# Kernel tuning notes

Hardware: AMD Instinct MI355X
Metric: run time of the kernel (lower is better)

Reference implementation:

```python
import jax, jax.numpy as jnp
import numpy as np

HEAD_DIM = 256
HIDDEN = 2560
NUM_HEADS = 8
NUM_KV_HEADS = 4
INPUT_DIM = HIDDEN * 2
B, S = 2, 2048


def rotate_half(x):
    x1, x2 = x[..., : x.shape[-1] // 2], x[..., x.shape[-1] // 2 :]
    return jnp.concatenate((-x2, x1), axis=-1)


def setup_inputs() -> dict:
    key = jax.random.key(0)
    ks = jax.random.split(key, 6)
    hidden_states = jax.random.normal(ks[0], (B, S, INPUT_DIM), dtype=jnp.float32)
    # causal additive mask (0 on/below diagonal, large negative above)
    causal = jnp.tril(jnp.ones((S, S), dtype=bool))
    attention_mask = jnp.where(causal, 0.0, -1e9).astype(jnp.float32)
    attention_mask = jnp.broadcast_to(attention_mask[None, None], (B, 1, S, S))
    position_ids = jnp.broadcast_to(jnp.arange(S, dtype=jnp.int32)[None], (B, S))
    sc = 1.0 / np.sqrt(INPUT_DIM)
    Wq = jax.random.normal(ks[1], (NUM_HEADS * HEAD_DIM, INPUT_DIM), dtype=jnp.float32) * sc
    Wk = jax.random.normal(ks[2], (NUM_KV_HEADS * HEAD_DIM, INPUT_DIM), dtype=jnp.float32) * sc
    Wv = jax.random.normal(ks[3], (NUM_KV_HEADS * HEAD_DIM, INPUT_DIM), dtype=jnp.float32) * sc
    Wo = jax.random.normal(ks[4], (HIDDEN, NUM_HEADS * HEAD_DIM), dtype=jnp.float32) * (1.0 / np.sqrt(NUM_HEADS * HEAD_DIM))
    return {"hidden_states": hidden_states, "attention_mask": attention_mask,
            "position_ids": position_ids, "Wq": Wq, "Wk": Wk, "Wv": Wv, "Wo": Wo}


def reference(hidden_states, attention_mask, position_ids, Wq, Wk, Wv, Wo):
    bsz, q_len, _ = hidden_states.shape
    groups = NUM_HEADS // NUM_KV_HEADS
    q = (hidden_states @ Wq.T).reshape(bsz, q_len, NUM_HEADS, HEAD_DIM).transpose(0, 2, 1, 3)
    k = (hidden_states @ Wk.T).reshape(bsz, q_len, NUM_KV_HEADS, HEAD_DIM).transpose(0, 2, 1, 3)
    v = (hidden_states @ Wv.T).reshape(bsz, q_len, NUM_KV_HEADS, HEAD_DIM).transpose(0, 2, 1, 3)
    # RoPE (uses position_ids[0], matching the torch module)
    inv_freq = 1.0 / (10000.0 ** (jnp.arange(0, HEAD_DIM, 2, dtype=jnp.float32) / HEAD_DIM))
    freqs = position_ids[0].astype(jnp.float32)[:, None] * inv_freq[None, :]  # [S, D/2]
    emb = jnp.concatenate((freqs, freqs), axis=-1)  # [S, D]
    cos = jnp.cos(emb)[None, None].astype(q.dtype)
    sin = jnp.sin(emb)[None, None].astype(q.dtype)
    q = q * cos + rotate_half(q) * sin
    k = k * cos + rotate_half(k) * sin
    # GQA: repeat kv heads
    k = jnp.repeat(k, groups, axis=1)  # [B, H, S, D]
    v = jnp.repeat(v, groups, axis=1)
    scores = jnp.einsum("bhqd,bhkd->bhqk", q, k) / np.sqrt(HEAD_DIM)
    scores = scores + attention_mask
    attn = jax.nn.softmax(scores.astype(jnp.float32), axis=-1).astype(q.dtype)
    out = jnp.einsum("bhqk,bhkd->bhqd", attn, v)
    out = out.transpose(0, 2, 1, 3).reshape(bsz, q_len, NUM_HEADS * HEAD_DIM)
    return out @ Wo.T
```

## Files before the change

### kernel.cpp

```cpp
#include <hip/hip_runtime.h>
#include <hip/hip_bf16.h>
#include <cstdint>
#include <cstddef>

typedef __bf16 bf16;
typedef bf16 bf16x4 __attribute__((ext_vector_type(4)));
typedef bf16 bf16x8 __attribute__((ext_vector_type(8)));
typedef float f32x4 __attribute__((ext_vector_type(4)));

#define HEAD_DIM 256
#define NHEADS 8
#define NKV 4
#define BATCH 2
#define SEQ 2048
#define IND 5120
#define HID 2560
#define ROWS (BATCH*SEQ)
#define NQKV 4096
#define CHUNKS_PER_BH 80

__device__ __forceinline__ f32x4 mfma16(bf16x8 a, bf16x8 b, f32x4 c) {
  return __builtin_amdgcn_mfma_f32_16x16x32_bf16(a, b, c, 0, 0, 0);
}

__global__ void cast_all(const float* __restrict__ hs, const float* __restrict__ wq,
                         const float* __restrict__ wk, const float* __restrict__ wv,
                         const float* __restrict__ wo,
                         bf16* __restrict__ dst01, bf16* __restrict__ dwo) {
  long i = ((long)blockIdx.x * 256 + threadIdx.x) * 8;
  const float* src; bf16* dst;
  if (i < 20971520L)      { src = hs + i;              dst = dst01 + i; }
  else if (i < 31457280L) { src = wq + (i - 20971520); dst = dst01 + i; }
  else if (i < 36700160L) { src = wk + (i - 31457280); dst = dst01 + i; }
  else if (i < 41943040L) { src = wv + (i - 36700160); dst = dst01 + i; }
  else                    { src = wo + (i - 41943040); dst = dwo + (i - 41943040); }
  float4 a = *(const float4*)(src);
  float4 b = *(const float4*)(src + 4);
  bf16x8 o;
  o[0] = (bf16)a.x; o[1] = (bf16)a.y; o[2] = (bf16)a.z; o[3] = (bf16)a.w;
  o[4] = (bf16)b.x; o[5] = (bf16)b.y; o[6] = (bf16)b.z; o[7] = (bf16)b.w;
  *(bf16x8*)dst = o;
}

template<typename OutT>
__global__ __launch_bounds__(512, 2) void gemm_pipe(const bf16* __restrict__ A,
                                                    const bf16* __restrict__ B,
                                                    OutT* __restrict__ C,
                                                    int M, int N, int K) {
  extern __shared__ bf16 smem[];
  const int tid = threadIdx.x;
  const int lane = tid & 63, w = tid >> 6;
  const int wm = w >> 2, wn = w & 3;
  const int l15 = lane & 15, lg = lane >> 4;
  const int gx = gridDim.x;
  const int nwg = gx * gridDim.y;
  const int id = blockIdx.y * gx + blockIdx.x;
  const int nid = (id & 7) * (nwg >> 3) + (id >> 3);
  const int m0 = (nid / gx) * 256, n0 = (nid % gx) * 256;
  const int NT = K >> 5;

  auto stage = [&](int slot, int kt) {
    bf16* sl = smem + slot * 16384;
    #pragma unroll
    for (int i = 0; i < 2; ++i) {
      int cid = i * 512 + tid;
      int sch = (cid & 3) ^ ((cid >> 3) & 3);
      __builtin_amdgcn_global_load_lds(
        (const __attribute__((address_space(1))) void*)(A + (size_t)(m0 + (cid >> 2)) * K + kt * 32 + sch * 8),
        (__attribute__((address_space(3))) void*)(sl + cid * 8), 16, 0, 0);
    }
    #pragma unroll
    for (int i = 0; i < 2; ++i) {
      int cid = i * 512 + tid;
      int sch = (cid & 3) ^ ((cid >> 3) & 3);
      __builtin_amdgcn_global_load_lds(
        (const __attribute__((address_space(1))) void*)(B + (size_t)(n0 + (cid >> 2)) * K + kt * 32 + sch * 8),
        (__attribute__((address_space(3))) void*)(sl + 8192 + cid * 8), 16, 0, 0);
    }
  };

  const int ach = lg ^ ((l15 >> 1) & 3);
  const int aoff = ((wm * 128 + l15) * 4 + ach) * 8;
  const int boff = 8192 + ((wn * 64 + l15) * 4 + ach) * 8;

  auto read_slot = [&](const bf16* sl, bf16x8 (&a)[8], bf16x8 (&b)[4]) {
    #pragma unroll
    for (int mi = 0; mi < 8; ++mi) a[mi] = *(const bf16x8*)&sl[aoff + mi * 512];
    #pragma unroll
    for (int ni = 0; ni < 4; ++ni) b[ni] = *(const bf16x8*)&sl[boff + ni * 512];
  };

  f32x4 acc[8][4] = {};
  auto domfma = [&](bf16x8 (&a)[8], bf16x8 (&b)[4]) {
    __builtin_amdgcn_s_setprio(1);
    #pragma unroll
    for (int ni = 0; ni < 4; ++ni)
      #pragma unroll
      for (int mi = 0; mi < 8; ++mi)
        acc[mi][ni] = mfma16(a[mi], b[ni], acc[mi][ni]);
    __builtin_amdgcn_s_setprio(0);
  };

  bf16x8 aE[8], bE[4], aO[8], bO[4];
  stage(0, 0); stage(1, 1); stage(2, 2);
  asm volatile("s_waitcnt vmcnt(8)" ::: "memory");
  __builtin_amdgcn_s_barrier();
  __builtin_amdgcn_sched_barrier(0);
  read_slot(smem, aE, bE);

  int t = 0;
  for (; t < NT - 2; t += 2) {
    asm volatile("s_waitcnt vmcnt(4)" ::: "memory");
    __builtin_amdgcn_s_barrier();
    __builtin_amdgcn_sched_barrier(0);
    read_slot(smem + ((t + 1) & 3) * 16384, aO, bO);
    { int kt = t + 3; if (kt > NT - 1) kt = NT - 1; stage((t + 3) & 3, kt); }
    domfma(aE, bE);
    asm volatile("s_waitcnt vmcnt(4)" ::: "memory");
    __builtin_amdgcn_s_barrier();
    __builtin_amdgcn_sched_barrier(0);
    read_slot(smem + ((t + 2) & 3) * 16384, aE, bE);
    { int kt = t + 4; if (kt > NT - 1) kt = NT - 1; stage((t + 4) & 3, kt); }
    domfma(aO, bO);
  }
  asm volatile("s_waitcnt vmcnt(4)" ::: "memory");
  __builtin_amdgcn_s_barrier();
  __builtin_amdgcn_sched_barrier(0);
  read_slot(smem + ((NT - 1) & 3) * 16384, aO, bO);
  domfma(aE, bE);
  domfma(aO, bO);

  #pragma unroll
  for (int mi = 0; mi < 8; ++mi)
    #pragma unroll
    for (int ni = 0; ni < 4; ++ni) {
      int row = m0 + wm * 128 + mi * 16 + lg * 4;
      int col = n0 + wn * 64 + ni * 16 + l15;
      #pragma unroll
      for (int r = 0; r < 4; ++r)
        C[(size_t)(row + r) * N + col] = (OutT)acc[mi][ni][r];
    }
}

__global__ void rope_reorder(const bf16* __restrict__ QKV,
                             bf16* __restrict__ Qr, bf16* __restrict__ Kr) {
  const int row = blockIdx.x;
  const int slot = blockIdx.y;
  const int d = threadIdx.x;
  const int b = row >> 11, s = row & 2047;
  const bool isq = slot < 8;
  const int col0 = isq ? slot * HEAD_DIM : 2048 + (slot - 8) * HEAD_DIM;
  float x1 = (float)QKV[(size_t)row * NQKV + col0 + d];
  float x2 = (float)QKV[(size_t)row * NQKV + col0 + d + 128];
  float invf = exp2f((float)d * (-13.287712379549449f / 128.0f));
  float fr = (float)s * invf;
  float sn, cs;
  sincosf(fr, &sn, &cs);
  bf16* dst = isq ? (Qr + ((size_t)(b * NHEADS + slot) * SEQ + s) * HEAD_DIM)
                  : (Kr + ((size_t)(b * NKV + (slot - 8)) * SEQ + s) * HEAD_DIM);
  dst[d]       = (bf16)(x1 * cs - x2 * sn);
  dst[d + 128] = (bf16)(x2 * cs + x1 * sn);
}

__global__ void v_transpose(const bf16* __restrict__ QKV, bf16* __restrict__ VT) {
  __shared__ bf16 tile[64][66];
  const int bkv = blockIdx.y;
  const int b = bkv >> 2, kv = bkv & 3;
  const int st = blockIdx.x & 31, dt = blockIdx.x >> 5;
  const int s0 = st * 64, d0 = dt * 64;
  const int tj = threadIdx.x & 63, ti = threadIdx.x >> 6;
  for (int i = ti; i < 64; i += 4)
    tile[i][tj] = QKV[(size_t)(b * SEQ + s0 + i) * NQKV + 3072 + kv * HEAD_DIM + d0 + tj];
  __syncthreads();
  for (int i = ti; i < 64; i += 4)
    VT[((size_t)bkv * HEAD_DIM + d0 + i) * SEQ + s0 + tj] = tile[tj][i];
}

__global__ __launch_bounds__(256) void flash_attn(const bf16* __restrict__ Q,
                                                  const bf16* __restrict__ Kp,
                                                  const bf16* __restrict__ VT,
                                                  bf16* __restrict__ Opart,
                                                  float* __restrict__ ML) {
  __shared__ bf16 Ks[64 * 256];
  __shared__ bf16 Vs[256 * 64];
  __shared__ bf16 pbuf[4][16][80];

  const int tid = threadIdx.x, lane = tid & 63, w = tid >> 6;
  const int l15 = lane & 15, lg = lane >> 4;

  const int cid = blockIdx.x;
  const int bh = cid / CHUNKS_PER_BH;
  const int c  = cid - bh * CHUNKS_PER_BH;
  int qt, ki;
  if (c < 8)       { qt = c;                 ki = 0; }
  else if (c < 24) { qt = 8  + ((c - 8) >> 1);  ki = (c - 8)  & 1; }
  else if (c < 48) { qt = 16 + (c - 24) / 3;    ki = (c - 24) % 3; }
  else             { qt = 24 + ((c - 48) >> 2); ki = (c - 48) & 3; }
  const int kb0 = ki * 8;
  const int kb1 = min(kb0 + 8, qt + 1);

  const int b = bh >> 3, h = bh & 7, kvh = h >> 1;
  const int bkv = b * NKV + kvh;
  const int q0 = qt * 64 + w * 16;

  const bf16* Qb = Q + ((size_t)bh * SEQ + q0) * HEAD_DIM;
  bf16x8 qf[8];
  #pragma unroll
  for (int dc = 0; dc < 8; ++dc)
    qf[dc] = *(const bf16x8*)&Qb[l15 * HEAD_DIM + dc * 32 + lg * 8];

  f32x4 oacc[16] = {};
  float m = -1e30f, l = 0.f;

  const bf16* Ksrc = Kp + (size_t)bkv * SEQ * HEAD_DIM;
  const bf16* Vsrc = VT + (size_t)bkv * HEAD_DIM * SEQ;

  for (int kb = kb0; kb < kb1; ++kb) {
    const int kbase = kb * 64;
    __syncthreads();
    #pragma unroll
    for (int i = 0; i < 8; ++i) {
      int id = i * 256 + tid;
      int row = id >> 5, ch = id & 31;
      int sc = ch ^ (row & 7);
      __builtin_amdgcn_global_load_lds(
          (const __attribute__((address_space(1))) void*)(Ksrc + (size_t)(kbase + row) * HEAD_DIM + sc * 8),
          (__attribute__((address_space(3))) void*)(Ks + id * 8), 16, 0, 0);
    }
    #pragma unroll
    for (int i = 0; i < 8; ++i) {
      int id = i * 256 + tid;
      int row = id >> 3, ch = id & 7;
      int sc = ch ^ (row & 7);
      __builtin_amdgcn_global_load_lds(
          (const __attribute__((address_space(1))) void*)(Vsrc + (size_t)row * SEQ + kbase + sc * 8),
          (__attribute__((address_space(3))) void*)(Vs + id * 8), 16, 0, 0);
    }
    __syncthreads();

    f32x4 sacc[4] = {};
    #pragma unroll
    for (int j = 0; j < 4; ++j) {
      const bf16* kl = &Ks[(j * 16 + l15) * HEAD_DIM];
      #pragma unroll
      for (int dc = 0; dc < 8; ++dc) {
        int ch = (dc * 4 + lg) ^ (l15 & 7);
        bf16x8 kf = *(const bf16x8*)&kl[ch * 8];
        sacc[j] = mfma16(kf, qf[dc], sacc[j]);
      }
    }

    float px[4][4];
    const bool need_mask = (kbase + 63 > q0);
    #pragma unroll
    for (int j = 0; j < 4; ++j)
      #pragma unroll
      for (int r = 0; r < 4; ++r) {
        float v = sacc[j][r] * 0.0625f;
        if (need_mask) {
          int kcol = kbase + j * 16 + lg * 4 + r;
          v = (kcol <= q0 + l15) ? v : -1e30f;
        }
        px[j][r] = v;
      }

    float mx = px[0][0];
    #pragma unroll
    for (int j = 0; j < 4; ++j)
      #pragma unroll
      for (int r = 0; r < 4; ++r) mx = fmaxf(mx, px[j][r]);
    mx = fmaxf(mx, __shfl_xor(mx, 16));
    mx = fmaxf(mx, __shfl_xor(mx, 32));
    float mnew = fmaxf(m, mx);
    float alpha = __expf(m - mnew);
    m = mnew;
    float s = 0.f;
    #pragma unroll
    for (int j = 0; j < 4; ++j) {
      bf16x4 pk;
      #pragma unroll
      for (int r = 0; r < 4; ++r) {
        float e = __expf(px[j][r] - mnew);
        s += e;
        pk[r] = (bf16)e;
      }
      *(bf16x4*)&pbuf[w][l15][j * 16 + lg * 4] = pk;
    }
    s += __shfl_xor(s, 16);
    s += __shfl_xor(s, 32);
    l = l * alpha + s;

    float ar[4];
    #pragma unroll
    for (int r = 0; r < 4; ++r) ar[r] = __shfl(alpha, lg * 4 + r);
    #pragma unroll
    for (int ni = 0; ni < 16; ++ni)
      #pragma unroll
      for (int r = 0; r < 4; ++r) oacc[ni][r] *= ar[r];

    bf16x8 pa0 = *(const bf16x8*)&pbuf[w][l15][lg * 8];
    bf16x8 pa1 = *(const bf16x8*)&pbuf[w][l15][32 + lg * 8];
    #pragma unroll
    for (int ni = 0; ni < 16; ++ni) {
      const bf16* vb = &Vs[(ni * 16 + l15) * 64];
      int c0 = lg ^ (l15 & 7);
      int c1 = (4 + lg) ^ (l15 & 7);
      bf16x8 v0 = *(const bf16x8*)&vb[c0 * 8];
      bf16x8 v1 = *(const bf16x8*)&vb[c1 * 8];
      oacc[ni] = mfma16(pa0, v0, oacc[ni]);
      oacc[ni] = mfma16(pa1, v1, oacc[ni]);
    }
  }

  bf16* Ob = Opart + ((size_t)cid * 64 + w * 16) * HEAD_DIM;
  #pragma unroll
  for (int ni = 0; ni < 16; ++ni)
    #pragma unroll
    for (int r = 0; r < 4; ++r)
      Ob[(size_t)(lg * 4 + r) * HEAD_DIM + ni * 16 + l15] = (bf16)oacc[ni][r];
  if (lg == 0) {
    ML[((size_t)cid * 64 + w * 16 + l15) * 2]     = m;
    ML[((size_t)cid * 64 + w * 16 + l15) * 2 + 1] = l;
  }
}

__global__ __launch_bounds__(256) void flash_merge(const bf16* __restrict__ Opart,
                                                   const float* __restrict__ ML,
                                                   bf16* __restrict__ AO) {
  const int bh = blockIdx.x, qt = blockIdx.y;
  const int b = bh >> 3, h = bh & 7;
  int cbase, nc;
  if (qt < 8)       { cbase = qt;                nc = 1; }
  else if (qt < 16) { cbase = 8  + 2 * (qt - 8);  nc = 2; }
  else if (qt < 24) { cbase = 24 + 3 * (qt - 16); nc = 3; }
  else              { cbase = 48 + 4 * (qt - 24); nc = 4; }
  const int cid0 = bh * CHUNKS_PER_BH + cbase;

  const int tid = threadIdx.x;
  const int row = tid >> 2, dseg = (tid & 3) * 64;

  float mi[4], li[4];
  float M = -1e30f;
  for (int i = 0; i < nc; ++i) {
    mi[i] = ML[((size_t)(cid0 + i) * 64 + row) * 2];
    li[i] = ML[((size_t)(cid0 + i) * 64 + row) * 2 + 1];
    M = fmaxf(M, mi[i]);
  }
  float wgt[4], L = 0.f;
  for (int i = 0; i < nc; ++i) {
    wgt[i] = __expf(mi[i] - M);
    L += li[i] * wgt[i];
  }
  const float inv = 1.0f / L;

  bf16* dst = AO + ((size_t)(b * SEQ + qt * 64 + row)) * 2048 + h * HEAD_DIM + dseg;
  for (int dv = 0; dv < 8; ++dv) {
    float acc[8] = {};
    for (int i = 0; i < nc; ++i) {
      bf16x8 o = *(const bf16x8*)&Opart[((size_t)(cid0 + i) * 64 + row) * HEAD_DIM + dseg + dv * 8];
      #pragma unroll
      for (int e = 0; e < 8; ++e) acc[e] += wgt[i] * (float)o[e];
    }
    bf16x8 ov;
    #pragma unroll
    for (int e = 0; e < 8; ++e) ov[e] = (bf16)(acc[e] * inv);
    *(bf16x8*)&dst[dv * 8] = ov;
  }
}

extern "C" void kernel_launch(void* const* d_in, const int* in_sizes, int n_in,
                              void* d_out, int out_size, void* d_ws, size_t ws_size,
                              hipStream_t stream) {
  const float* hs = (const float*)d_in[0];
  const float* Wq = (const float*)d_in[3];
  const float* Wk = (const float*)d_in[4];
  const float* Wv = (const float*)d_in[5];
  const float* Wo = (const float*)d_in[6];
  float* out = (float*)d_out;

  char* ws = (char*)d_ws;
  bf16* hsb  = (bf16*)(ws);
  bf16* wqkv = (bf16*)(ws + 41943040);
  bf16* qkv  = (bf16*)(ws + 83886080);
  bf16* qr   = (bf16*)(ws + 117440512);
  bf16* kr   = (bf16*)(ws + 134217728);
  bf16* vt   = (bf16*)(ws + 142606336);
  bf16* ao   = (bf16*)(ws + 150994944);
  bf16* wob  = (bf16*)(ws + 167772160);
  bf16*  opart = (bf16*)(ws);
  float* ml    = (float*)(ws + 41943040);

  hipFuncSetAttribute((const void*)&gemm_pipe<bf16>,  hipFuncAttributeMaxDynamicSharedMemorySize, 131072);
  hipFuncSetAttribute((const void*)&gemm_pipe<float>, hipFuncAttributeMaxDynamicSharedMemorySize, 131072);

  cast_all<<<23040, 256, 0, stream>>>(hs, Wq, Wk, Wv, Wo, (bf16*)ws, wob);

  gemm_pipe<bf16><<<dim3(NQKV / 256, ROWS / 256), 512, 131072, stream>>>(hsb, wqkv, qkv, ROWS, NQKV, IND);

  rope_reorder<<<dim3(ROWS, 12), 128, 0, stream>>>(qkv, qr, kr);
  v_transpose<<<dim3(128, BATCH * NKV), 256, 0, stream>>>(qkv, vt);

  flash_attn<<<dim3(16 * CHUNKS_PER_BH), 256, 0, stream>>>(qr, kr, vt, opart, ml);
  flash_merge<<<dim3(16, 32), 256, 0, stream>>>(opart, ml, ao);

  gemm_pipe<float><<<dim3(HID / 256, ROWS / 256), 512, 131072, stream>>>(ao, wob, out, ROWS, HID, 2048);
}
```

Measured before the change: 410.1 us.

## Restructure GEMM main loop into fine-grained phases interleaving loads and MFMAs

```diff
diff --git a/kernel.cpp b/kernel.cpp
--- a/kernel.cpp
+++ b/kernel.cpp
@@ -57,78 +57,77 @@
   const int id = blockIdx.y * gx + blockIdx.x;
   const int nid = (id & 7) * (nwg >> 3) + (id >> 3);
   const int m0 = (nid / gx) * 256, n0 = (nid % gx) * 256;
-  const int NT = K >> 5;
-
-  auto stage = [&](int slot, int kt) {
-    bf16* sl = smem + slot * 16384;
+  const int NT = K >> 6;
+  const int NI = NT >> 1;
+
+  auto stage_unit = [&](int tile, int su) {
+    const bf16* Mat = (su & 1) ? B : A;
+    const int base0 = (su & 1) ? n0 : m0;
+    bf16* dst = smem + (tile & 1) * 32768 + (su >> 1) * 16384 + (su & 1) * 8192;
+    const int kbase = tile * 64 + (su >> 1) * 32;
     #pragma unroll
     for (int i = 0; i < 2; ++i) {
-      int cid = i * 512 + tid;
-      int sch = (cid & 3) ^ ((cid >> 3) & 3);
+      int c = i * 512 + tid;
+      int row = c >> 2, sub = c & 3;
+      int sch = sub ^ ((row >> 1) & 3);
       __builtin_amdgcn_global_load_lds(
-        (const __attribute__((address_space(1))) void*)(A + (size_t)(m0 + (cid >> 2)) * K + kt * 32 + sch * 8),
-        (__attribute__((address_space(3))) void*)(sl + cid * 8), 16, 0, 0);
-    }
-    #pragma unroll
-    for (int i = 0; i < 2; ++i) {
-      int cid = i * 512 + tid;
-      int sch = (cid & 3) ^ ((cid >> 3) & 3);
-      __builtin_amdgcn_global_load_lds(
-        (const __attribute__((address_space(1))) void*)(B + (size_t)(n0 + (cid >> 2)) * K + kt * 32 + sch * 8),
-        (__attribute__((address_space(3))) void*)(sl + 8192 + cid * 8), 16, 0, 0);
+        (const __attribute__((address_space(1))) void*)(Mat + (size_t)(base0 + row) * K + kbase + sch * 8),
+        (__attribute__((address_space(3))) void*)(dst + c * 8), 16, 0, 0);
     }
   };
 
   const int ach = lg ^ ((l15 >> 1) & 3);
-  const int aoff = ((wm * 128 + l15) * 4 + ach) * 8;
-  const int boff = 8192 + ((wn * 64 + l15) * 4 + ach) * 8;
-
-  auto read_slot = [&](const bf16* sl, bf16x8 (&a)[8], bf16x8 (&b)[4]) {
-    #pragma unroll
-    for (int mi = 0; mi < 8; ++mi) a[mi] = *(const bf16x8*)&sl[aoff + mi * 512];
-    #pragma unroll
-    for (int ni = 0; ni < 4; ++ni) b[ni] = *(const bf16x8*)&sl[boff + ni * 512];
+  const int aoffb = ((wm * 128 + l15) * 4 + ach) * 8;
+  const int boffb = ((wn * 64 + l15) * 4 + ach) * 8;
+
+  f32x4 acc[8][4] = {};
+  bf16x8 af[8];
+
+  auto phase = [&](const bf16* rb, int qn, int stile, int ssu, bool do_vm) {
+    if (qn == 0) {
+      #pragma unroll
+      for (int mi = 0; mi < 8; ++mi) af[mi] = *(const bf16x8*)&rb[aoffb + mi * 512];
+    }
+    bf16x8 b0 = *(const bf16x8*)&rb[8192 + boffb + (qn * 2) * 512];
+    bf16x8 b1 = *(const bf16x8*)&rb[8192 + boffb + (qn * 2 + 1) * 512];
+    stage_unit(stile, ssu);
+    if (do_vm) asm volatile("s_waitcnt vmcnt(8)" ::: "memory");
+    asm volatile("s_barrier" ::: "memory");
+    asm volatile("s_waitcnt lgkmcnt(0)" ::: "memory");
+    __builtin_amdgcn_sched_barrier(0);
+    __builtin_amdgcn_s_setprio(1);
+    #pragma unroll
+    for (int mi = 0; mi < 8; ++mi) {
+      acc[mi][qn * 2]     = mfma16(af[mi], b0, acc[mi][qn * 2]);
+      acc[mi][qn * 2 + 1] = mfma16(af[mi], b1, acc[mi][qn * 2 + 1]);
+    }
+    __builtin_amdgcn_s_setprio(0);
+    asm volatile("s_barrier" ::: "memory");
   };
 
-  f32x4 acc[8][4] = {};
-  auto domfma = [&](bf16x8 (&a)[8], bf16x8 (&b)[4]) {
-    __builtin_amdgcn_s_setprio(1);
-    #pragma unroll
-    for (int ni = 0; ni < 4; ++ni)
-      #pragma unroll
-      for (int mi = 0; mi < 8; ++mi)
-        acc[mi][ni] = mfma16(a[mi], b[ni], acc[mi][ni]);
-    __builtin_amdgcn_s_setprio(0);
-  };
-
-  bf16x8 aE[8], bE[4], aO[8], bO[4];
-  stage(0, 0); stage(1, 1); stage(2, 2);
+  stage_unit(0, 0); stage_unit(0, 1); stage_unit(0, 2); stage_unit(0, 3);
+  stage_unit(1, 0); stage_unit(1, 1);
   asm volatile("s_waitcnt vmcnt(8)" ::: "memory");
-  __builtin_amdgcn_s_barrier();
-  __builtin_amdgcn_sched_barrier(0);
-  read_slot(smem, aE, bE);
-
-  int t = 0;
-  for (; t < NT - 2; t += 2) {
-    asm volatile("s_waitcnt vmcnt(4)" ::: "memory");
-    __builtin_amdgcn_s_barrier();
-    __builtin_amdgcn_sched_barrier(0);
-    read_slot(smem + ((t + 1) & 3) * 16384, aO, bO);
-    { int kt = t + 3; if (kt > NT - 1) kt = NT - 1; stage((t + 3) & 3, kt); }
-    domfma(aE, bE);
-    asm volatile("s_waitcnt vmcnt(4)" ::: "memory");
-    __builtin_amdgcn_s_barrier();
-    __builtin_amdgcn_sched_barrier(0);
-    read_slot(smem + ((t + 2) & 3) * 16384, aE, bE);
-    { int kt = t + 4; if (kt > NT - 1) kt = NT - 1; stage((t + 4) & 3, kt); }
-    domfma(aO, bO);
-  }
-  asm volatile("s_waitcnt vmcnt(4)" ::: "memory");
-  __builtin_amdgcn_s_barrier();
-  __builtin_amdgcn_sched_barrier(0);
-  read_slot(smem + ((NT - 1) & 3) * 16384, aO, bO);
-  domfma(aE, bE);
-  domfma(aO, bO);
+  asm volatile("s_barrier" ::: "memory");
+
+  for (int I = 0; I < NI; ++I) {
+    const int t = 2 * I;
+    const int t2 = (t + 2 < NT) ? t + 2 : NT - 1;
+    const int t3 = (t + 3 < NT) ? t + 3 : NT - 1;
+    const bf16* rb0k0 = smem;
+    const bf16* rb0k1 = smem + 16384;
+    const bf16* rb1k0 = smem + 32768;
+    const bf16* rb1k1 = smem + 49152;
+    phase(rb0k0, 0, t + 1, 2, false);
+    phase(rb0k0, 1, t + 1, 3, true);
+    phase(rb0k1, 0, t2, 0, false);
+    phase(rb0k1, 1, t2, 1, true);
+    phase(rb1k0, 0, t2, 2, false);
+    phase(rb1k0, 1, t2, 3, true);
+    phase(rb1k1, 0, t3, 0, false);
+    phase(rb1k1, 1, t3, 1, true);
+  }
+  asm volatile("s_waitcnt vmcnt(0)" ::: "memory");
 
   #pragma unroll
   for (int mi = 0; mi < 8; ++mi)
```

Result: no change. 412.3 us (+0.5%).

## Double-buffer K/V tiles in flash attention with 128-row query tiles

Applied to the files above, without the earlier changes.

```diff
diff --git a/kernel.cpp b/kernel.cpp
--- a/kernel.cpp
+++ b/kernel.cpp
@@ -17,7 +17,7 @@
 #define HID 2560
 #define ROWS (BATCH*SEQ)
 #define NQKV 4096
-#define CHUNKS_PER_BH 80
+#define CHUNKS_PER_BH 40
 
 __device__ __forceinline__ f32x4 mfma16(bf16x8 a, bf16x8 b, f32x4 c) {
   return __builtin_amdgcn_mfma_f32_16x16x32_bf16(a, b, c, 0, 0, 0);
@@ -176,15 +176,12 @@
     VT[((size_t)bkv * HEAD_DIM + d0 + i) * SEQ + s0 + tj] = tile[tj][i];
 }
 
-__global__ __launch_bounds__(256) void flash_attn(const bf16* __restrict__ Q,
-                                                  const bf16* __restrict__ Kp,
-                                                  const bf16* __restrict__ VT,
-                                                  bf16* __restrict__ Opart,
-                                                  float* __restrict__ ML) {
-  __shared__ bf16 Ks[64 * 256];
-  __shared__ bf16 Vs[256 * 64];
-  __shared__ bf16 pbuf[4][16][80];
-
+__global__ __launch_bounds__(512, 2) void flash_attn(const bf16* __restrict__ Q,
+                                                     const bf16* __restrict__ Kp,
+                                                     const bf16* __restrict__ VT,
+                                                     bf16* __restrict__ Opart,
+                                                     float* __restrict__ ML) {
+  extern __shared__ bf16 fsm[];
   const int tid = threadIdx.x, lane = tid & 63, w = tid >> 6;
   const int l15 = lane & 15, lg = lane >> 4;
 
@@ -192,16 +189,16 @@
   const int bh = cid / CHUNKS_PER_BH;
   const int c  = cid - bh * CHUNKS_PER_BH;
   int qt, ki;
-  if (c < 8)       { qt = c;                 ki = 0; }
-  else if (c < 24) { qt = 8  + ((c - 8) >> 1);  ki = (c - 8)  & 1; }
-  else if (c < 48) { qt = 16 + (c - 24) / 3;    ki = (c - 24) % 3; }
-  else             { qt = 24 + ((c - 48) >> 2); ki = (c - 48) & 3; }
+  if (c < 4)       { qt = c;                  ki = 0; }
+  else if (c < 12) { qt = 4  + ((c - 4) >> 1);  ki = (c - 4)  & 1; }
+  else if (c < 24) { qt = 8  + (c - 12) / 3;    ki = (c - 12) % 3; }
+  else             { qt = 12 + ((c - 24) >> 2); ki = (c - 24) & 3; }
   const int kb0 = ki * 8;
-  const int kb1 = min(kb0 + 8, qt + 1);
+  const int kb1 = min(kb0 + 8, 2 * qt + 2);
 
   const int b = bh >> 3, h = bh & 7, kvh = h >> 1;
   const int bkv = b * NKV + kvh;
-  const int q0 = qt * 64 + w * 16;
+  const int q0 = qt * 128 + w * 16;
 
   const bf16* Qb = Q + ((size_t)bh * SEQ + q0) * HEAD_DIM;
   bf16x8 qf[8];
@@ -214,34 +211,52 @@
 
   const bf16* Ksrc = Kp + (size_t)bkv * SEQ * HEAD_DIM;
   const bf16* Vsrc = VT + (size_t)bkv * HEAD_DIM * SEQ;
-
-  for (int kb = kb0; kb < kb1; ++kb) {
+  bf16* pb = fsm + 65536 + w * 16 * 80;
+
+  auto stage = [&](int kb, int bi) {
     const int kbase = kb * 64;
-    __syncthreads();
-    #pragma unroll
-    for (int i = 0; i < 8; ++i) {
-      int id = i * 256 + tid;
+    bf16* kd = fsm + bi * 16384;
+    bf16* vd = fsm + 32768 + bi * 16384;
+    #pragma unroll
+    for (int i = 0; i < 4; ++i) {
+      int id = i * 512 + tid;
       int row = id >> 5, ch = id & 31;
       int sc = ch ^ (row & 7);
       __builtin_amdgcn_global_load_lds(
           (const __attribute__((address_space(1))) void*)(Ksrc + (size_t)(kbase + row) * HEAD_DIM + sc * 8),
-          (__attribute__((address_space(3))) void*)(Ks + id * 8), 16, 0, 0);
-    }
-    #pragma unroll
-    for (int i = 0; i < 8; ++i) {
-      int id = i * 256 + tid;
+          (__attribute__((address_space(3))) void*)(kd + id * 8), 16, 0, 0);
+    }
+    #pragma unroll
+    for (int i = 0; i < 4; ++i) {
+      int id = i * 512 + tid;
       int row = id >> 3, ch = id & 7;
       int sc = ch ^ (row & 7);
       __builtin_amdgcn_global_load_lds(
           (const __attribute__((address_space(1))) void*)(Vsrc + (size_t)row * SEQ + kbase + sc * 8),
-          (__attribute__((address_space(3))) void*)(Vs + id * 8), 16, 0, 0);
-    }
-    __syncthreads();
+          (__attribute__((address_space(3))) void*)(vd + id * 8), 16, 0, 0);
+    }
+  };
+
+  stage(kb0, 0);
+
+  for (int kb = kb0; kb < kb1; ++kb) {
+    const int bufc = (kb - kb0) & 1;
+    const int kbase = kb * 64;
+    if (kb + 1 < kb1) {
+      stage(kb + 1, bufc ^ 1);
+      asm volatile("s_waitcnt vmcnt(8)" ::: "memory");
+    } else {
+      asm volatile("s_waitcnt vmcnt(0)" ::: "memory");
+    }
+    asm volatile("s_barrier" ::: "memory");
+    const bf16* Ksc = fsm + bufc * 16384;
+    const bf16* Vsc = fsm + 32768 + bufc * 16384;
 
     f32x4 sacc[4] = {};
+    __builtin_amdgcn_s_setprio(1);
     #pragma unroll
     for (int j = 0; j < 4; ++j) {
-      const bf16* kl = &Ks[(j * 16 + l15) * HEAD_DIM];
+      const bf16* kl = &Ksc[(j * 16 + l15) * HEAD_DIM];
       #pragma unroll
       for (int dc = 0; dc < 8; ++dc) {
         int ch = (dc * 4 + lg) ^ (l15 & 7);
@@ -249,6 +264,7 @@
         sacc[j] = mfma16(kf, qf[dc], sacc[j]);
       }
     }
+    __builtin_amdgcn_s_setprio(0);
 
     float px[4][4];
     const bool need_mask = (kbase + 63 > q0);
@@ -284,7 +300,7 @@
         s += e;
         pk[r] = (bf16)e;
       }
-      *(bf16x4*)&pbuf[w][l15][j * 16 + lg * 4] = pk;
+      *(bf16x4*)&pb[l15 * 80 + j * 16 + lg * 4] = pk;
     }
     s += __shfl_xor(s, 16);
     s += __shfl_xor(s, 32);
@@ -298,11 +314,12 @@
       #pragma unroll
       for (int r = 0; r < 4; ++r) oacc[ni][r] *= ar[r];
 
-    bf16x8 pa0 = *(const bf16x8*)&pbuf[w][l15][lg * 8];
-    bf16x8 pa1 = *(const bf16x8*)&pbuf[w][l15][32 + lg * 8];
+    bf16x8 pa0 = *(const bf16x8*)&pb[l15 * 80 + lg * 8];
+    bf16x8 pa1 = *(const bf16x8*)&pb[l15 * 80 + 32 + lg * 8];
+    __builtin_amdgcn_s_setprio(1);
     #pragma unroll
     for (int ni = 0; ni < 16; ++ni) {
-      const bf16* vb = &Vs[(ni * 16 + l15) * 64];
+      const bf16* vb = &Vsc[(ni * 16 + l15) * 64];
       int c0 = lg ^ (l15 & 7);
       int c1 = (4 + lg) ^ (l15 & 7);
       bf16x8 v0 = *(const bf16x8*)&vb[c0 * 8];
@@ -310,17 +327,19 @@
       oacc[ni] = mfma16(pa0, v0, oacc[ni]);
       oacc[ni] = mfma16(pa1, v1, oacc[ni]);
     }
-  }
-
-  bf16* Ob = Opart + ((size_t)cid * 64 + w * 16) * HEAD_DIM;
+    __builtin_amdgcn_s_setprio(0);
+    asm volatile("s_barrier" ::: "memory");
+  }
+
+  bf16* Ob = Opart + ((size_t)cid * 128 + w * 16) * HEAD_DIM;
   #pragma unroll
   for (int ni = 0; ni < 16; ++ni)
     #pragma unroll
     for (int r = 0; r < 4; ++r)
       Ob[(size_t)(lg * 4 + r) * HEAD_DIM + ni * 16 + l15] = (bf16)oacc[ni][r];
   if (lg == 0) {
-    ML[((size_t)cid * 64 + w * 16 + l15) * 2]     = m;
-    ML[((size_t)cid * 64 + w * 16 + l15) * 2 + 1] = l;
+    ML[((size_t)cid * 128 + w * 16 + l15) * 2]     = m;
+    ML[((size_t)cid * 128 + w * 16 + l15) * 2 + 1] = l;
   }
 }
 
@@ -329,21 +348,23 @@
                                                    bf16* __restrict__ AO) {
   const int bh = blockIdx.x, qt = blockIdx.y;
   const int b = bh >> 3, h = bh & 7;
-  int cbase, nc;
-  if (qt < 8)       { cbase = qt;                nc = 1; }
-  else if (qt < 16) { cbase = 8  + 2 * (qt - 8);  nc = 2; }
-  else if (qt < 24) { cbase = 24 + 3 * (qt - 16); nc = 3; }
-  else              { cbase = 48 + 4 * (qt - 24); nc = 4; }
+  const int g = qt >> 2;
+  const int nc = g + 1;
+  int cbase;
+  if (g == 0)      cbase = qt;
+  else if (g == 1) cbase = 4  + 2 * (qt - 4);
+  else if (g == 2) cbase = 12 + 3 * (qt - 8);
+  else             cbase = 24 + 4 * (qt - 12);
   const int cid0 = bh * CHUNKS_PER_BH + cbase;
 
   const int tid = threadIdx.x;
-  const int row = tid >> 2, dseg = (tid & 3) * 64;
+  const int row = tid >> 1, dh = (tid & 1) * 128;
 
   float mi[4], li[4];
   float M = -1e30f;
   for (int i = 0; i < nc; ++i) {
-    mi[i] = ML[((size_t)(cid0 + i) * 64 + row) * 2];
-    li[i] = ML[((size_t)(cid0 + i) * 64 + row) * 2 + 1];
+    mi[i] = ML[((size_t)(cid0 + i) * 128 + row) * 2];
+    li[i] = ML[((size_t)(cid0 + i) * 128 + row) * 2 + 1];
     M = fmaxf(M, mi[i]);
   }
   float wgt[4], L = 0.f;
@@ -353,11 +374,11 @@
   }
   const float inv = 1.0f / L;
 
-  bf16* dst = AO + ((size_t)(b * SEQ + qt * 64 + row)) * 2048 + h * HEAD_DIM + dseg;
-  for (int dv = 0; dv < 8; ++dv) {
+  bf16* dst = AO + ((size_t)(b * SEQ + qt * 128 + row)) * 2048 + h * HEAD_DIM + dh;
+  for (int dv = 0; dv < 16; ++dv) {
     float acc[8] = {};
     for (int i = 0; i < nc; ++i) {
-      bf16x8 o = *(const bf16x8*)&Opart[((size_t)(cid0 + i) * 64 + row) * HEAD_DIM + dseg + dv * 8];
+      bf16x8 o = *(const bf16x8*)&Opart[((size_t)(cid0 + i) * 128 + row) * HEAD_DIM + dh + dv * 8];
       #pragma unroll
       for (int e = 0; e < 8; ++e) acc[e] += wgt[i] * (float)o[e];
     }
@@ -392,6 +413,7 @@
 
   hipFuncSetAttribute((const void*)&gemm_pipe<bf16>,  hipFuncAttributeMaxDynamicSharedMemorySize, 131072);
   hipFuncSetAttribute((const void*)&gemm_pipe<float>, hipFuncAttributeMaxDynamicSharedMemorySize, 131072);
+  hipFuncSetAttribute((const void*)&flash_attn,       hipFuncAttributeMaxDynamicSharedMemorySize, 151552);
 
   cast_all<<<23040, 256, 0, stream>>>(hs, Wq, Wk, Wv, Wo, (bf16*)ws, wob);
 
@@ -400,8 +422,8 @@
   rope_reorder<<<dim3(ROWS, 12), 128, 0, stream>>>(qkv, qr, kr);
   v_transpose<<<dim3(128, BATCH * NKV), 256, 0, stream>>>(qkv, vt);
 
-  flash_attn<<<dim3(16 * CHUNKS_PER_BH), 256, 0, stream>>>(qr, kr, vt, opart, ml);
-  flash_merge<<<dim3(16, 32), 256, 0, stream>>>(opart, ml, ao);
+  flash_attn<<<dim3(16 * CHUNKS_PER_BH), 512, 151552, stream>>>(qr, kr, vt, opart, ml);
+  flash_merge<<<dim3(16, 16), 256, 0, stream>>>(opart, ml, ao);
 
   gemm_pipe<float><<<dim3(HID / 256, ROWS / 256), 512, 131072, stream>>>(ao, wob, out, ROWS, HID, 2048);
 }
```

After: 372.1 us. 1.1x faster.

## Add 128x128 GEMM for output projection and restructure flash-attention K/V loading

Applied to the files above, without the earlier changes.

```diff
diff --git a/kernel.cpp b/kernel.cpp
--- a/kernel.cpp
+++ b/kernel.cpp
@@ -135,6 +135,106 @@
     #pragma unroll
     for (int ni = 0; ni < 4; ++ni) {
       int row = m0 + wm * 128 + mi * 16 + lg * 4;
+      int col = n0 + wn * 64 + ni * 16 + l15;
+      #pragma unroll
+      for (int r = 0; r < 4; ++r)
+        C[(size_t)(row + r) * N + col] = (OutT)acc[mi][ni][r];
+    }
+}
+
+template<typename OutT>
+__global__ __launch_bounds__(256, 2) void gemm_pipe128(const bf16* __restrict__ A,
+                                                       const bf16* __restrict__ B,
+                                                       OutT* __restrict__ C,
+                                                       int M, int N, int K) {
+  extern __shared__ bf16 smem[];
+  const int tid = threadIdx.x;
+  const int lane = tid & 63, w = tid >> 6;
+  const int wm = w >> 1, wn = w & 1;
+  const int l15 = lane & 15, lg = lane >> 4;
+  const int gx = gridDim.x;
+  const int nwg = gx * gridDim.y;
+  const int id = blockIdx.y * gx + blockIdx.x;
+  const int nid = (id & 7) * (nwg >> 3) + (id >> 3);
+  const int m0 = (nid / gx) * 128, n0 = (nid % gx) * 128;
+  const int NT = K >> 5;
+
+  auto stage = [&](int slot, int kt) {
+    bf16* sl = smem + slot * 8192;
+    #pragma unroll
+    for (int i = 0; i < 2; ++i) {
+      int cid = i * 256 + tid;
+      int sch = (cid & 3) ^ ((cid >> 3) & 3);
+      __builtin_amdgcn_global_load_lds(
+        (const __attribute__((address_space(1))) void*)(A + (size_t)(m0 + (cid >> 2)) * K + kt * 32 + sch * 8),
+        (__attribute__((address_space(3))) void*)(sl + cid * 8), 16, 0, 0);
+    }
+    #pragma unroll
+    for (int i = 0; i < 2; ++i) {
+      int cid = i * 256 + tid;
+      int sch = (cid & 3) ^ ((cid >> 3) & 3);
+      __builtin_amdgcn_global_load_lds(
+        (const __attribute__((address_space(1))) void*)(B + (size_t)(n0 + (cid >> 2)) * K + kt * 32 + sch * 8),
+        (__attribute__((address_space(3))) void*)(sl + 4096 + cid * 8), 16, 0, 0);
+    }
+  };
+
+  const int ach = lg ^ ((l15 >> 1) & 3);
+  const int aoff = ((wm * 64 + l15) * 4 + ach) * 8;
+  const int boff = 4096 + ((wn * 64 + l15) * 4 + ach) * 8;
+
+  auto read_slot = [&](const bf16* sl, bf16x8 (&a)[4], bf16x8 (&b)[4]) {
+    #pragma unroll
+    for (int mi = 0; mi < 4; ++mi) a[mi] = *(const bf16x8*)&sl[aoff + mi * 512];
+    #pragma unroll
+    for (int ni = 0; ni < 4; ++ni) b[ni] = *(const bf16x8*)&sl[boff + ni * 512];
+  };
+
+  f32x4 acc[4][4] = {};
+  auto domfma = [&](bf16x8 (&a)[4], bf16x8 (&b)[4]) {
+    __builtin_amdgcn_s_setprio(1);
+    #pragma unroll
+    for (int ni = 0; ni < 4; ++ni)
+      #pragma unroll
+      for (int mi = 0; mi < 4; ++mi)
+        acc[mi][ni] = mfma16(a[mi], b[ni], acc[mi][ni]);
+    __builtin_amdgcn_s_setprio(0);
+  };
+
+  bf16x8 aE[4], bE[4], aO[4], bO[4];
+  stage(0, 0); stage(1, 1); stage(2, 2);
+  asm volatile("s_waitcnt vmcnt(8)" ::: "memory");
+  __builtin_amdgcn_s_barrier();
+  __builtin_amdgcn_sched_barrier(0);
+  read_slot(smem, aE, bE);
+
+  int t = 0;
+  for (; t < NT - 2; t += 2) {
+    asm volatile("s_waitcnt vmcnt(4)" ::: "memory");
+    __builtin_amdgcn_s_barrier();
+    __builtin_amdgcn_sched_barrier(0);
+    read_slot(smem + ((t + 1) & 3) * 8192, aO, bO);
+    { int kt = t + 3; if (kt > NT - 1) kt = NT - 1; stage((t + 3) & 3, kt); }
+    domfma(aE, bE);
+    asm volatile("s_waitcnt vmcnt(4)" ::: "memory");
+    __builtin_amdgcn_s_barrier();
+    __builtin_amdgcn_sched_barrier(0);
+    read_slot(smem + ((t + 2) & 3) * 8192, aE, bE);
+    { int kt = t + 4; if (kt > NT - 1) kt = NT - 1; stage((t + 4) & 3, kt); }
+    domfma(aO, bO);
+  }
+  asm volatile("s_waitcnt vmcnt(4)" ::: "memory");
+  __builtin_amdgcn_s_barrier();
+  __builtin_amdgcn_sched_barrier(0);
+  read_slot(smem + ((NT - 1) & 3) * 8192, aO, bO);
+  domfma(aE, bE);
+  domfma(aO, bO);
+
+  #pragma unroll
+  for (int mi = 0; mi < 4; ++mi)
+    #pragma unroll
+    for (int ni = 0; ni < 4; ++ni) {
+      int row = m0 + wm * 64 + mi * 16 + lg * 4;
       int col = n0 + wn * 64 + ni * 16 + l15;
       #pragma unroll
       for (int r = 0; r < 4; ++r)
@@ -182,7 +282,6 @@
                                                   bf16* __restrict__ Opart,
                                                   float* __restrict__ ML) {
   __shared__ bf16 Ks[64 * 256];
-  __shared__ bf16 Vs[256 * 64];
   __shared__ bf16 pbuf[4][16][80];
 
   const int tid = threadIdx.x, lane = tid & 63, w = tid >> 6;
@@ -215,30 +314,35 @@
   const bf16* Ksrc = Kp + (size_t)bkv * SEQ * HEAD_DIM;
   const bf16* Vsrc = VT + (size_t)bkv * HEAD_DIM * SEQ;
 
-  for (int kb = kb0; kb < kb1; ++kb) {
-    const int kbase = kb * 64;
-    __syncthreads();
+  bf16x8 vk[8];
+  auto kload = [&](int kb) {
     #pragma unroll
     for (int i = 0; i < 8; ++i) {
       int id = i * 256 + tid;
       int row = id >> 5, ch = id & 31;
-      int sc = ch ^ (row & 7);
-      __builtin_amdgcn_global_load_lds(
-          (const __attribute__((address_space(1))) void*)(Ksrc + (size_t)(kbase + row) * HEAD_DIM + sc * 8),
-          (__attribute__((address_space(3))) void*)(Ks + id * 8), 16, 0, 0);
-    }
+      vk[i] = *(const bf16x8*)&Ksrc[(size_t)(kb * 64 + row) * HEAD_DIM + ch * 8];
+    }
+  };
+  auto kwrite = [&]() {
     #pragma unroll
     for (int i = 0; i < 8; ++i) {
       int id = i * 256 + tid;
-      int row = id >> 3, ch = id & 7;
-      int sc = ch ^ (row & 7);
-      __builtin_amdgcn_global_load_lds(
-          (const __attribute__((address_space(1))) void*)(Vsrc + (size_t)row * SEQ + kbase + sc * 8),
-          (__attribute__((address_space(3))) void*)(Vs + id * 8), 16, 0, 0);
-    }
-    __syncthreads();
+      int row = id >> 5, ch = id & 31;
+      *(bf16x8*)&Ks[(size_t)(row * 32 + (ch ^ (row & 7))) * 8] = vk[i];
+    }
+  };
+
+  kload(kb0);
+  kwrite();
+  __syncthreads();
+
+  for (int kb = kb0; kb < kb1; ++kb) {
+    const int kbase = kb * 64;
+    const bool more = (kb + 1 < kb1);
+    if (more) kload(kb + 1);
 
     f32x4 sacc[4] = {};
+    __builtin_amdgcn_s_setprio(1);
     #pragma unroll
     for (int j = 0; j < 4; ++j) {
       const bf16* kl = &Ks[(j * 16 + l15) * HEAD_DIM];
@@ -249,6 +353,8 @@
         sacc[j] = mfma16(kf, qf[dc], sacc[j]);
       }
     }
+    __builtin_amdgcn_s_setprio(0);
+    asm volatile("s_barrier" ::: "memory");
 
     float px[4][4];
     const bool need_mask = (kbase + 63 > q0);
@@ -290,6 +396,8 @@
     s += __shfl_xor(s, 32);
     l = l * alpha + s;
 
+    if (more) kwrite();
+
     float ar[4];
     #pragma unroll
     for (int r = 0; r < 4; ++r) ar[r] = __shfl(alpha, lg * 4 + r);
@@ -300,16 +408,17 @@
 
     bf16x8 pa0 = *(const bf16x8*)&pbuf[w][l15][lg * 8];
     bf16x8 pa1 = *(const bf16x8*)&pbuf[w][l15][32 + lg * 8];
+    __builtin_amdgcn_s_setprio(1);
     #pragma unroll
     for (int ni = 0; ni < 16; ++ni) {
-      const bf16* vb = &Vs[(ni * 16 + l15) * 64];
-      int c0 = lg ^ (l15 & 7);
-      int c1 = (4 + lg) ^ (l15 & 7);
-      bf16x8 v0 = *(const bf16x8*)&vb[c0 * 8];
-      bf16x8 v1 = *(const bf16x8*)&vb[c1 * 8];
+      const bf16* vb = &Vsrc[(size_t)(ni * 16 + l15) * SEQ + kbase + lg * 8];
+      bf16x8 v0 = *(const bf16x8*)&vb[0];
+      bf16x8 v1 = *(const bf16x8*)&vb[32];
       oacc[ni] = mfma16(pa0, v0, oacc[ni]);
       oacc[ni] = mfma16(pa1, v1, oacc[ni]);
     }
+    __builtin_amdgcn_s_setprio(0);
+    __syncthreads();
   }
 
   bf16* Ob = Opart + ((size_t)cid * 64 + w * 16) * HEAD_DIM;
@@ -390,8 +499,8 @@
   bf16*  opart = (bf16*)(ws);
   float* ml    = (float*)(ws + 41943040);
 
-  hipFuncSetAttribute((const void*)&gemm_pipe<bf16>,  hipFuncAttributeMaxDynamicSharedMemorySize, 131072);
-  hipFuncSetAttribute((const void*)&gemm_pipe<float>, hipFuncAttributeMaxDynamicSharedMemorySize, 131072);
+  hipFuncSetAttribute((const void*)&gemm_pipe<bf16>,     hipFuncAttributeMaxDynamicSharedMemorySize, 131072);
+  hipFuncSetAttribute((const void*)&gemm_pipe128<float>, hipFuncAttributeMaxDynamicSharedMemorySize, 65536);
 
   cast_all<<<23040, 256, 0, stream>>>(hs, Wq, Wk, Wv, Wo, (bf16*)ws, wob);
 
@@ -403,5 +512,5 @@
   flash_attn<<<dim3(16 * CHUNKS_PER_BH), 256, 0, stream>>>(qr, kr, vt, opart, ml);
   flash_merge<<<dim3(16, 32), 256, 0, stream>>>(opart, ml, ao);
 
-  gemm_pipe<float><<<dim3(HID / 256, ROWS / 256), 512, 131072, stream>>>(ao, wob, out, ROWS, HID, 2048);
-}
+  gemm_pipe128<float><<<dim3(HID / 128, ROWS / 128), 256, 65536, stream>>>(ao, wob, out, ROWS, HID, 2048);
+}
```

New measurement: 619.1 us. 1.51x slower.
